# Optimization experiments

Measured on AMD Instinct MI355X. Metric: run time of the kernel, lower is better.

Reference implementation:

```python
import jax, jax.numpy as jnp
import numpy as np

B, S, D, N = 8, 4096, 1024, 16
EPS = 1e-6


def setup_inputs() -> dict:
    key = jax.random.key(0)
    ks = jax.random.split(key, 6)
    s = 1.0 / np.sqrt(D)
    return {
        "x": jax.random.normal(ks[0], (B, S, D), dtype=jnp.float32),
        "W_lambda": jax.random.uniform(ks[1], (N, D), jnp.float32, -s, s),
        "b_lambda": jnp.full((N,), 2.0, dtype=jnp.float32),  # nn.init.constant_(bias, 2.0)
        "W_B": jax.random.uniform(ks[2], (N, D), jnp.float32, -s, s),
        "W_C": jax.random.uniform(ks[3], (D, N), jnp.float32, -1.0 / np.sqrt(N), 1.0 / np.sqrt(N)),
        "W_gate": jax.random.uniform(ks[4], (D, D), jnp.float32, -s, s),
        "rms_weight": jnp.ones((D,), dtype=jnp.float32),
    }


def reference(x, W_lambda, b_lambda, W_B, W_C, W_gate, rms_weight):
    # Input-dependent decay and input projection, computed for all timesteps at once
    lam = jax.nn.sigmoid(jnp.einsum("bsd,nd->bsn", x, W_lambda) + b_lambda)  # (B,S,N)
    Bx = jnp.einsum("bsd,nd->bsn", x, W_B)  # (B,S,N)

    def step(h, inp):
        l_t, b_t = inp
        h = l_t * h + b_t  # h_t = lambda_t * h_{t-1} + B_t x_t
        return h, h

    h0 = jnp.zeros((x.shape[0], W_B.shape[0]), dtype=x.dtype)
    _, hs = jax.lax.scan(step, h0, (jnp.swapaxes(lam, 0, 1), jnp.swapaxes(Bx, 0, 1)))
    hs = jnp.swapaxes(hs, 0, 1)  # (B,S,N)

    y = jnp.einsum("bsn,dn->bsd", hs, W_C)  # C @ h_t
    gate = jax.nn.sigmoid(jnp.einsum("bsd,ed->bse", x, W_gate))
    y = gate * y
    # RMSNorm
    rms = jax.lax.rsqrt(jnp.mean(y * y, axis=-1, keepdims=True) + EPS)
    return y * rms * rms_weight
```

## Files before the change

### kernel.cpp

```cpp
#include <hip/hip_runtime.h>

#define DD 1024
#define NN 16
#define SS 4096
#define BBATCH 8
#define TOK (BBATCH*SS)

typedef __attribute__((ext_vector_type(8))) __bf16 bf16x8;
typedef __attribute__((ext_vector_type(4))) float f32x4;
typedef unsigned int u32;
typedef unsigned long long u64;

__device__ __forceinline__ void async16(void* lds, const void* g) {
  __builtin_amdgcn_global_load_lds(
      (const __attribute__((address_space(1))) u32*)(u64)(g),
      (__attribute__((address_space(3))) u32*)(u32)(u64)(lds), 16, 0, 0);
}

__device__ __forceinline__ float sigmoidf_(float v) {
  return 1.f / (1.f + __expf(-v));
}

__global__ void k_cvt(const float* __restrict__ in, __bf16* __restrict__ out, int n8) {
  int i = blockIdx.x * blockDim.x + threadIdx.x;
  if (i >= n8) return;
  const float4* in4 = (const float4*)in;
  float4 a = in4[(u64)i * 2 + 0];
  float4 b = in4[(u64)i * 2 + 1];
  bf16x8 o;
  o[0] = (__bf16)a.x; o[1] = (__bf16)a.y; o[2] = (__bf16)a.z; o[3] = (__bf16)a.w;
  o[4] = (__bf16)b.x; o[5] = (__bf16)b.y; o[6] = (__bf16)b.z; o[7] = (__bf16)b.w;
  *(bf16x8*)(out + (u64)i * 8) = o;
}

__global__ __launch_bounds__(256)
void k_proj(const __bf16* __restrict__ xb, const __bf16* __restrict__ wp,
            const float* __restrict__ b_lambda,
            float* __restrict__ lam, float* __restrict__ bx) {
  __shared__ __align__(16) __bf16 sA[128 * 32];
  __shared__ __align__(16) __bf16 sB[32 * 32];
  int tid = threadIdx.x;
  int lane = tid & 63, w = tid >> 6;
  int tok0 = blockIdx.x * 128;
  u64 aSrc[2];
#pragma unroll
  for (int q = 0; q < 2; ++q) {
    int u = q * 256 + tid;
    int row = u >> 2, slot = (u & 3) ^ (row & 3);
    aSrc[q] = (u64)((const char*)xb + ((u64)(tok0 + row) * DD + slot * 8) * 2);
  }
  u64 bSrc;
  {
    int u = tid;
    int row = u >> 2, slot = (u & 3) ^ (row & 3);
    bSrc = (u64)((const char*)wp + ((u64)row * DD + slot * 8) * 2);
  }
  f32x4 acc[2][2] = {};
  int r15 = lane & 15, kg = lane >> 4;
  for (int kt = 0; kt < DD / 32; ++kt) {
#pragma unroll
    for (int q = 0; q < 2; ++q)
      async16((char*)sA + (q * 256 + w * 64) * 16, (const void*)(aSrc[q] + kt * 64));
    if (tid < 128)
      async16((char*)sB + w * 1024, (const void*)(bSrc + kt * 64));
    __syncthreads();
    bf16x8 bfr[2];
#pragma unroll
    for (int nt = 0; nt < 2; ++nt) {
      int brow = nt * 16 + r15;
      bfr[nt] = *(const bf16x8*)((const char*)sB + brow * 64 + ((kg ^ (brow & 3)) << 4));
    }
#pragma unroll
    for (int mt = 0; mt < 2; ++mt) {
      int arow = w * 32 + mt * 16 + r15;
      bf16x8 af = *(const bf16x8*)((const char*)sA + arow * 64 + ((kg ^ (arow & 3)) << 4));
#pragma unroll
      for (int nt = 0; nt < 2; ++nt)
        acc[mt][nt] = __builtin_amdgcn_mfma_f32_16x16x32_bf16(af, bfr[nt], acc[mt][nt], 0, 0, 0);
    }
    __syncthreads();
  }
#pragma unroll
  for (int mt = 0; mt < 2; ++mt)
#pragma unroll
    for (int nt = 0; nt < 2; ++nt)
#pragma unroll
      for (int r = 0; r < 4; ++r) {
        int token = tok0 + w * 32 + mt * 16 + kg * 4 + r;
        int j = nt * 16 + r15;
        float v = acc[mt][nt][r];
        if (j < 16) lam[token * NN + j] = sigmoidf_(v + b_lambda[j]);
        else        bx[token * NN + (j - 16)] = v;
      }
}

__global__ __launch_bounds__(256)
void k_scan(const float* __restrict__ lam, const float* __restrict__ bx,
            float* __restrict__ hs) {
  int b = blockIdx.x >> 4, n = blockIdx.x & 15;
  int t = threadIdx.x;
  const int CH = SS / 256;
  float lv[CH], bv[CH];
  int base = (b * SS + t * CH) * NN + n;
  float a = 1.f, bacc = 0.f;
#pragma unroll
  for (int i = 0; i < CH; ++i) {
    lv[i] = lam[base + i * NN];
    bv[i] = bx[base + i * NN];
    bacc = lv[i] * bacc + bv[i];
    a *= lv[i];
  }
  __shared__ float As[2][256], Bs[2][256];
  As[0][t] = a; Bs[0][t] = bacc;
  __syncthreads();
  int cur = 0;
  for (int off = 1; off < 256; off <<= 1) {
    float a2 = As[cur][t], b2 = Bs[cur][t];
    if (t >= off) {
      float ap = As[cur][t - off], bp = Bs[cur][t - off];
      b2 = b2 + a2 * bp;
      a2 = a2 * ap;
    }
    As[cur ^ 1][t] = a2; Bs[cur ^ 1][t] = b2;
    cur ^= 1;
    __syncthreads();
  }
  float h = (t == 0) ? 0.f : Bs[cur][t - 1];
#pragma unroll
  for (int i = 0; i < CH; ++i) {
    h = lv[i] * h + bv[i];
    hs[base + i * NN] = h;
  }
}

__global__ __launch_bounds__(256, 3)
void k_gemm(const __bf16* __restrict__ xb, const __bf16* __restrict__ wg,
            const float* __restrict__ hs, const float* __restrict__ wc,
            float* __restrict__ out) {
  __shared__ __align__(16) union {
    struct { __bf16 A[128 * 32]; __bf16 B[128 * 32]; } st;
    struct { float hsl[128 * 16]; float wcl[128 * 16]; } ep;
  } sm;
  int tid = threadIdx.x, lane = tid & 63, w = tid >> 6;
  int bid = blockIdx.x;
  int swz = (bid & 7) * 256 + (bid >> 3);
  int m = swz >> 3, n = swz & 7;
  int tok0 = m * 128, n0 = n * 128;
  int r15 = lane & 15, kg = lane >> 4;
  int wr = w >> 1, wcq = w & 1;
  u64 aSrc[2], bSrc[2];
#pragma unroll
  for (int q = 0; q < 2; ++q) {
    int u = q * 256 + tid;
    int row = u >> 2, slot = (u & 3) ^ (row & 3);
    aSrc[q] = (u64)((const char*)xb + ((u64)(tok0 + row) * DD + slot * 8) * 2);
    bSrc[q] = (u64)((const char*)wg + ((u64)(n0 + row) * DD + slot * 8) * 2);
  }
  f32x4 acc[4][4] = {};
  for (int kt = 0; kt < DD / 32; ++kt) {
#pragma unroll
    for (int q = 0; q < 2; ++q) {
      async16((char*)sm.st.A + (q * 256 + w * 64) * 16, (const void*)(aSrc[q] + kt * 64));
      async16((char*)sm.st.B + (q * 256 + w * 64) * 16, (const void*)(bSrc[q] + kt * 64));
    }
    __syncthreads();
    bf16x8 af[4];
#pragma unroll
    for (int mt = 0; mt < 4; ++mt) {
      int arow = wr * 64 + mt * 16 + r15;
      af[mt] = *(const bf16x8*)((const char*)sm.st.A + arow * 64 + ((kg ^ (arow & 3)) << 4));
    }
#pragma unroll
    for (int nt = 0; nt < 4; ++nt) {
      int brow = wcq * 64 + nt * 16 + r15;
      bf16x8 bfr = *(const bf16x8*)((const char*)sm.st.B + brow * 64 + ((kg ^ (brow & 3)) << 4));
#pragma unroll
      for (int mt = 0; mt < 4; ++mt)
        acc[mt][nt] = __builtin_amdgcn_mfma_f32_16x16x32_bf16(af[mt], bfr, acc[mt][nt], 0, 0, 0);
    }
    __syncthreads();
  }
  for (int idx = tid; idx < 128 * 16; idx += 256)
    sm.ep.hsl[idx] = hs[(u64)tok0 * NN + idx];
  for (int idx = tid; idx < 128 * 16; idx += 256)
    sm.ep.wcl[idx] = wc[(u64)n0 * NN + idx];
  __syncthreads();
  f32x4 wcv[4][4];
#pragma unroll
  for (int nt = 0; nt < 4; ++nt) {
    int j = wcq * 64 + nt * 16 + r15;
#pragma unroll
    for (int q = 0; q < 4; ++q)
      wcv[nt][q] = *(const f32x4*)(&sm.ep.wcl[j * 16 + q * 4]);
  }
#pragma unroll
  for (int mt = 0; mt < 4; ++mt)
#pragma unroll
    for (int r = 0; r < 4; ++r) {
      int i = wr * 64 + mt * 16 + kg * 4 + r;
      f32x4 hv[4];
#pragma unroll
      for (int q = 0; q < 4; ++q)
        hv[q] = *(const f32x4*)(&sm.ep.hsl[i * 16 + q * 4]);
#pragma unroll
      for (int nt = 0; nt < 4; ++nt) {
        f32x4 cv = hv[0] * wcv[nt][0];
        cv += hv[1] * wcv[nt][1];
        cv += hv[2] * wcv[nt][2];
        cv += hv[3] * wcv[nt][3];
        float cy = cv[0] + cv[1] + cv[2] + cv[3];
        float g = sigmoidf_(acc[mt][nt][r]);
        int j = wcq * 64 + nt * 16 + r15;
        out[(u64)(tok0 + i) * DD + n0 + j] = g * cy;
      }
    }
}

__global__ __launch_bounds__(256)
void k_norm(float* __restrict__ out, const float* __restrict__ rw) {
  int row = blockIdx.x * 4 + (threadIdx.x >> 6);
  int lane = threadIdx.x & 63;
  float4* p = (float4*)(out + (u64)row * DD);
  float4 v[4];
  float rs = 0.f;
#pragma unroll
  for (int e = 0; e < 4; ++e) {
    v[e] = p[e * 64 + lane];
    rs += v[e].x * v[e].x + v[e].y * v[e].y + v[e].z * v[e].z + v[e].w * v[e].w;
  }
#pragma unroll
  for (int msk = 1; msk < 64; msk <<= 1) rs += __shfl_xor(rs, msk, 64);
  float rstd = rsqrtf(rs * (1.f / DD) + 1e-6f);
  const float4* rwp = (const float4*)rw;
#pragma unroll
  for (int e = 0; e < 4; ++e) {
    float4 wv = rwp[e * 64 + lane];
    float4 o;
    o.x = v[e].x * rstd * wv.x;
    o.y = v[e].y * rstd * wv.y;
    o.z = v[e].z * rstd * wv.z;
    o.w = v[e].w * rstd * wv.w;
    p[e * 64 + lane] = o;
  }
}

extern "C" void kernel_launch(void* const* d_in, const int* in_sizes, int n_in,
                              void* d_out, int out_size, void* d_ws, size_t ws_size,
                              hipStream_t stream) {
  (void)in_sizes; (void)n_in; (void)out_size; (void)ws_size;
  const float* x        = (const float*)d_in[0];
  const float* W_lambda = (const float*)d_in[1];
  const float* b_lambda = (const float*)d_in[2];
  const float* W_B      = (const float*)d_in[3];
  const float* W_C      = (const float*)d_in[4];
  const float* W_gate   = (const float*)d_in[5];
  const float* rms_w    = (const float*)d_in[6];
  char* ws = (char*)d_ws;
  __bf16* xb  = (__bf16*)(ws + 0);
  __bf16* wg  = (__bf16*)(ws + 67108864);
  __bf16* wp  = (__bf16*)(ws + 69206016);
  float*  lam = (float*)(ws + 69271552);
  float*  bx  = (float*)(ws + 71368704);
  float*  hs  = (float*)(ws + 73465856);
  float*  out = (float*)d_out;

  k_cvt<<<TOK * DD / 8 / 256, 256, 0, stream>>>(x, xb, TOK * DD / 8);
  k_cvt<<<DD * DD / 8 / 256, 256, 0, stream>>>(W_gate, wg, DD * DD / 8);
  k_cvt<<<NN * DD / 8 / 256, 256, 0, stream>>>(W_lambda, wp, NN * DD / 8);
  k_cvt<<<NN * DD / 8 / 256, 256, 0, stream>>>(W_B, wp + NN * DD, NN * DD / 8);
  k_proj<<<TOK / 128, 256, 0, stream>>>(xb, wp, b_lambda, lam, bx);
  k_scan<<<BBATCH * NN, 256, 0, stream>>>(lam, bx, hs);
  k_gemm<<<(TOK / 128) * (DD / 128), 256, 0, stream>>>(xb, wg, hs, W_C, out);
  k_norm<<<TOK / 4, 256, 0, stream>>>(out, rms_w);
}
```

Before: 220.5 us.

## Enlarge gate GEMM tile to 256x256 with 4-stage async LDS pipeline

Rewrites the gate GEMM to use 256x256 tiles with 512 threads (8 waves) and a four-buffer ring of global_load_lds stages, kept three tiles ahead and synchronised with explicit vmcnt waits and raw barriers instead of a full sync around each single-buffered k-step. It also changes the LDS swizzle to XOR two row bit groups and raises wave priority around the MFMA block. The goal is to hide global load latency and raise arithmetic intensity per block. In exchange it uses 128KB of LDS and more accumulator registers per thread, which limits occupancy and leaves fewer blocks (512) to spread across the CUs.

```diff
diff --git a/kernel.cpp b/kernel.cpp
--- a/kernel.cpp
+++ b/kernel.cpp
@@ -133,75 +133,88 @@
   }
 }
 
-__global__ __launch_bounds__(256, 3)
+#define STG(kt, bi) do { u32 lb = (u32)(bi) * 32768u; u64 ko = (u64)(kt) * 64u;          \
+    async16(smc + lb + (u32)w * 1024u,              (const void*)(aAddr0 + ko));         \
+    async16(smc + lb + (u32)(8 + w) * 1024u,        (const void*)(aAddr1 + ko));         \
+    async16(smc + lb + 16384u + (u32)w * 1024u,     (const void*)(bAddr0 + ko));         \
+    async16(smc + lb + 16384u + (u32)(8 + w) * 1024u,(const void*)(bAddr1 + ko)); } while (0)
+
+__global__ __launch_bounds__(512, 2)
 void k_gemm(const __bf16* __restrict__ xb, const __bf16* __restrict__ wg,
             const float* __restrict__ hs, const float* __restrict__ wc,
             float* __restrict__ out) {
-  __shared__ __align__(16) union {
-    struct { __bf16 A[128 * 32]; __bf16 B[128 * 32]; } st;
-    struct { float hsl[128 * 16]; float wcl[128 * 16]; } ep;
-  } sm;
-  int tid = threadIdx.x, lane = tid & 63, w = tid >> 6;
+  __shared__ __align__(16) char smc[131072];
+  const int tid = threadIdx.x, lane = tid & 63, w = tid >> 6;
+  const int r15 = lane & 15, kg = lane >> 4;
+  const int wr = w >> 2, wcq = w & 3;
   int bid = blockIdx.x;
-  int swz = (bid & 7) * 256 + (bid >> 3);
-  int m = swz >> 3, n = swz & 7;
-  int tok0 = m * 128, n0 = n * 128;
-  int r15 = lane & 15, kg = lane >> 4;
-  int wr = w >> 1, wcq = w & 1;
-  u64 aSrc[2], bSrc[2];
-#pragma unroll
-  for (int q = 0; q < 2; ++q) {
-    int u = q * 256 + tid;
-    int row = u >> 2, slot = (u & 3) ^ (row & 3);
-    aSrc[q] = (u64)((const char*)xb + ((u64)(tok0 + row) * DD + slot * 8) * 2);
-    bSrc[q] = (u64)((const char*)wg + ((u64)(n0 + row) * DD + slot * 8) * 2);
-  }
-  f32x4 acc[4][4] = {};
-  for (int kt = 0; kt < DD / 32; ++kt) {
-#pragma unroll
-    for (int q = 0; q < 2; ++q) {
-      async16((char*)sm.st.A + (q * 256 + w * 64) * 16, (const void*)(aSrc[q] + kt * 64));
-      async16((char*)sm.st.B + (q * 256 + w * 64) * 16, (const void*)(bSrc[q] + kt * 64));
-    }
-    __syncthreads();
-    bf16x8 af[4];
-#pragma unroll
-    for (int mt = 0; mt < 4; ++mt) {
-      int arow = wr * 64 + mt * 16 + r15;
-      af[mt] = *(const bf16x8*)((const char*)sm.st.A + arow * 64 + ((kg ^ (arow & 3)) << 4));
-    }
+  int swz = (bid & 7) * 64 + (bid >> 3);
+  int m = swz >> 2, n = swz & 3;
+  const int tok0 = m * 256, n0 = n * 256;
+  const int sslot = (lane & 3) ^ ((lane >> 2) & 3) ^ ((lane >> 4) & 3);
+  const int rA0 = w * 16 + (lane >> 2);
+  const int rA1 = (8 + w) * 16 + (lane >> 2);
+  const u64 aAddr0 = (u64)(const char*)xb + (u64)(tok0 + rA0) * 2048 + (u32)sslot * 16;
+  const u64 aAddr1 = (u64)(const char*)xb + (u64)(tok0 + rA1) * 2048 + (u32)sslot * 16;
+  const u64 bAddr0 = (u64)(const char*)wg + (u64)(n0 + rA0) * 2048 + (u32)sslot * 16;
+  const u64 bAddr1 = (u64)(const char*)wg + (u64)(n0 + rA1) * 2048 + (u32)sslot * 16;
+
+  f32x4 acc[8][4] = {};
+
+  STG(0, 0); STG(1, 1); STG(2, 2);
+  asm volatile("s_waitcnt vmcnt(8)" ::: "memory");
+  __builtin_amdgcn_s_barrier();
+  __builtin_amdgcn_sched_barrier(0);
+
+  for (int t = 0; t < 32; ++t) {
+    if (t + 3 < 32) STG(t + 3, (t + 3) & 3);
+    const char* Ab = smc + (t & 3) * 32768;
+    const char* Bb = Ab + 16384;
+    bf16x8 af[8];
+#pragma unroll
+    for (int mt = 0; mt < 8; ++mt) {
+      int row = wr * 128 + mt * 16 + r15;
+      int sl = kg ^ (row & 3) ^ ((row >> 2) & 3);
+      af[mt] = *(const bf16x8*)(Ab + row * 64 + sl * 16);
+    }
+    __builtin_amdgcn_s_setprio(1);
 #pragma unroll
     for (int nt = 0; nt < 4; ++nt) {
       int brow = wcq * 64 + nt * 16 + r15;
-      bf16x8 bfr = *(const bf16x8*)((const char*)sm.st.B + brow * 64 + ((kg ^ (brow & 3)) << 4));
-#pragma unroll
-      for (int mt = 0; mt < 4; ++mt)
+      int sl = kg ^ (brow & 3) ^ ((brow >> 2) & 3);
+      bf16x8 bfr = *(const bf16x8*)(Bb + brow * 64 + sl * 16);
+#pragma unroll
+      for (int mt = 0; mt < 8; ++mt)
         acc[mt][nt] = __builtin_amdgcn_mfma_f32_16x16x32_bf16(af[mt], bfr, acc[mt][nt], 0, 0, 0);
     }
-    __syncthreads();
-  }
-  for (int idx = tid; idx < 128 * 16; idx += 256)
-    sm.ep.hsl[idx] = hs[(u64)tok0 * NN + idx];
-  for (int idx = tid; idx < 128 * 16; idx += 256)
-    sm.ep.wcl[idx] = wc[(u64)n0 * NN + idx];
+    __builtin_amdgcn_s_setprio(0);
+    if (t < 29)       asm volatile("s_waitcnt vmcnt(8)" ::: "memory");
+    else if (t == 29) asm volatile("s_waitcnt vmcnt(4)" ::: "memory");
+    else              asm volatile("s_waitcnt vmcnt(0)" ::: "memory");
+    __builtin_amdgcn_s_barrier();
+    __builtin_amdgcn_sched_barrier(0);
+  }
+
+  float* hsl = (float*)smc;
+  float* wcl = (float*)(smc + 16384);
+  for (int idx = tid; idx < 256 * 16; idx += 512) hsl[idx] = hs[(u64)tok0 * NN + idx];
+  for (int idx = tid; idx < 256 * 16; idx += 512) wcl[idx] = wc[(u64)n0 * NN + idx];
   __syncthreads();
   f32x4 wcv[4][4];
 #pragma unroll
   for (int nt = 0; nt < 4; ++nt) {
     int j = wcq * 64 + nt * 16 + r15;
 #pragma unroll
-    for (int q = 0; q < 4; ++q)
-      wcv[nt][q] = *(const f32x4*)(&sm.ep.wcl[j * 16 + q * 4]);
-  }
-#pragma unroll
-  for (int mt = 0; mt < 4; ++mt)
+    for (int q = 0; q < 4; ++q) wcv[nt][q] = *(const f32x4*)(wcl + j * 16 + q * 4);
+  }
+#pragma unroll
+  for (int mt = 0; mt < 8; ++mt)
 #pragma unroll
     for (int r = 0; r < 4; ++r) {
-      int i = wr * 64 + mt * 16 + kg * 4 + r;
+      int i = wr * 128 + mt * 16 + kg * 4 + r;
       f32x4 hv[4];
 #pragma unroll
-      for (int q = 0; q < 4; ++q)
-        hv[q] = *(const f32x4*)(&sm.ep.hsl[i * 16 + q * 4]);
+      for (int q = 0; q < 4; ++q) hv[q] = *(const f32x4*)(hsl + i * 16 + q * 4);
 #pragma unroll
       for (int nt = 0; nt < 4; ++nt) {
         f32x4 cv = hv[0] * wcv[nt][0];
@@ -270,6 +283,6 @@
   k_cvt<<<NN * DD / 8 / 256, 256, 0, stream>>>(W_B, wp + NN * DD, NN * DD / 8);
   k_proj<<<TOK / 128, 256, 0, stream>>>(xb, wp, b_lambda, lam, bx);
   k_scan<<<BBATCH * NN, 256, 0, stream>>>(lam, bx, hs);
-  k_gemm<<<(TOK / 128) * (DD / 128), 256, 0, stream>>>(xb, wg, hs, W_C, out);
+  k_gemm<<<(TOK / 256) * (DD / 256), 512, 0, stream>>>(xb, wg, hs, W_C, out);
   k_norm<<<TOK / 4, 256, 0, stream>>>(out, rms_w);
 }
```

Result: faster. 209.7 us (-4.9%).
